# Optimization experiments

Measured on AMD Instinct MI355X. Metric: run time of the kernel, lower is better.

## Reference

```python
import jax, jax.numpy as jnp
import numpy as np

B, T, C = 4, 1024, 768
NH = 12
HD = C // NH  # 64


def setup_inputs() -> dict:
    key = jax.random.key(0)
    k1, k2, k3, k4, k5 = jax.random.split(key, 5)
    s = 0.02
    return {
        "x": jax.random.normal(k1, (B, T, C), dtype=jnp.float32),
        "Wqkv": jax.random.normal(k2, (C, 3 * C), dtype=jnp.float32) * s,
        "bqkv": jax.random.normal(k3, (3 * C,), dtype=jnp.float32) * s,
        "Wproj": jax.random.normal(k4, (C, C), dtype=jnp.float32) * s,
        "bproj": jax.random.normal(k5, (C,), dtype=jnp.float32) * s,
        "start_pos": 0,
    }


def reference(x, Wqkv, bqkv, Wproj, bproj, start_pos):
    # Manual QKV projection (nn.Linear with weight stored as [in, out])
    Bq, Tq, Cq = x.shape
    qkv = x @ Wqkv + bqkv                       # [B, T, 3C]
    q, k, v = jnp.split(qkv, 3, axis=-1)
    q = q.reshape(Bq, Tq, NH, HD)
    k = k.reshape(Bq, Tq, NH, HD)
    v = v.reshape(Bq, Tq, NH, HD)
    # With start_pos=0 the KV-cache write+slice is an identity on k, v.
    att = jnp.einsum("bqhd,bkhd->bhqk", q, k) / jnp.sqrt(jnp.float32(HD))
    causal = jnp.tril(jnp.ones((Tq, Tq), dtype=bool))  # [T, T]
    att = jnp.where(causal[None, None], att, jnp.float32(-jnp.inf))
    att = jax.nn.softmax(att, axis=-1)
    out = jnp.einsum("bhqk,bkhd->bqhd", att, v).reshape(Bq, Tq, Cq)
    return out @ Wproj + bproj
```

## Files before the change

### kernel.cpp

```cpp
#include <hip/hip_runtime.h>


#define BB 4
#define TT 1024
#define CC 768
#define NHH 12
#define HDD 64
#define BHH (BB*NHH)

typedef unsigned short u16;
typedef __attribute__((ext_vector_type(8))) short bf16x8;
typedef __attribute__((ext_vector_type(4))) float f32x4;
typedef __attribute__((ext_vector_type(4))) int i32x4;

__device__ __forceinline__ u16 f2b(float f) {
  unsigned u = __float_as_uint(f);
  u += 0x7fffu + ((u >> 16) & 1u);
  return (u16)(u >> 16);
}
__device__ __forceinline__ unsigned packbf(float lo, float hi) {
  return (__float_as_uint(hi) & 0xffff0000u) | (__float_as_uint(lo) >> 16);
}

__device__ __forceinline__ void gload_lds16(const u16* g, u16* l) {
  __builtin_amdgcn_global_load_lds(
      (const __attribute__((address_space(1))) unsigned int*)g,
      (__attribute__((address_space(3))) unsigned int*)l, 16, 0, 0);
}

__device__ __forceinline__ void tr_body(const float* __restrict__ in, u16* __restrict__ out,
                                        int R, int Cc, int bx, int by, float (*tile)[33]) {
  int c0 = bx * 32, r0 = by * 32;
  int tx = threadIdx.x & 31, ty = threadIdx.x >> 5;
#pragma unroll
  for (int i = 0; i < 32; i += 8)
    tile[ty + i][tx] = in[(r0 + ty + i) * Cc + c0 + tx];
  __syncthreads();
#pragma unroll
  for (int i = 0; i < 32; i += 8)
    out[(c0 + ty + i) * R + r0 + tx] = f2b(tile[tx][ty + i]);
}

__global__ __launch_bounds__(256) void k_prep(const float* __restrict__ x, u16* __restrict__ xb,
                                              const float* __restrict__ Wqkv, u16* __restrict__ Wqkv_t,
                                              const float* __restrict__ Wproj, u16* __restrict__ Wproj_t) {
  __shared__ float tile[32][33];
  int bid = blockIdx.x;
  if (bid < 3072) {
    int i = bid * 256 + threadIdx.x;
    float4 v = ((const float4*)x)[i];
    ushort4 o;
    o.x = f2b(v.x); o.y = f2b(v.y); o.z = f2b(v.z); o.w = f2b(v.w);
    ((ushort4*)xb)[i] = o;
  } else if (bid < 3072 + 1728) {
    int tb = bid - 3072;
    tr_body(Wqkv, Wqkv_t, CC, 3 * CC, tb % 72, tb / 72, tile);
  } else {
    int tb = bid - 4800;
    tr_body(Wproj, Wproj_t, CC, CC, tb % 24, tb / 24, tile);
  }
}

#define GEMM_CORE64(A_, Bt_, m0_, n0_, SMEM)                                      \
  u16* As = (SMEM); u16* Bs = (SMEM) + 8192;                                      \
  int tid = threadIdx.x;                                                          \
  int wave = tid >> 6, lane = tid & 63, quad = lane >> 4, id16 = lane & 15;       \
  int wm = (wave & 1) * 64, wn = (wave >> 1) * 64;                                \
  int srow = tid >> 3;                                                            \
  int schunk = (tid & 7) ^ (srow & 7);                                            \
  const u16* ga = A_ + (m0_ + srow) * CC + schunk * 8;                            \
  const u16* gb = Bt_ + (n0_ + srow) * CC + schunk * 8;                           \
  int xk = id16 & 7;                                                              \
  int off0 = (quad ^ xk) * 8, off1 = ((4 + quad) ^ xk) * 8;                       \
  f32x4 acc[4][4];                                                                \
  _Pragma("unroll") for (int i = 0; i < 4; i++)                                   \
      _Pragma("unroll") for (int j = 0; j < 4; j++) acc[i][j] = (f32x4){0,0,0,0}; \
  for (int k0 = 0; k0 < CC; k0 += 64) {                                           \
    _Pragma("unroll") for (int i = 0; i < 4; i++) {                               \
      gload_lds16(ga + i * 32 * CC + k0, As + i * 2048 + tid * 8);                \
      gload_lds16(gb + i * 32 * CC + k0, Bs + i * 2048 + tid * 8);                \
    }                                                                             \
    __syncthreads();                                                              \
    bf16x8 af[4][2], bfr[4][2];                                                   \
    _Pragma("unroll") for (int i = 0; i < 4; i++) {                               \
      const u16* ar = As + (wm + i * 16 + id16) * 64;                             \
      af[i][0] = *(const bf16x8*)(ar + off0);                                     \
      af[i][1] = *(const bf16x8*)(ar + off1);                                     \
    }                                                                             \
    _Pragma("unroll") for (int j = 0; j < 4; j++) {                               \
      const u16* br = Bs + (wn + j * 16 + id16) * 64;                             \
      bfr[j][0] = *(const bf16x8*)(br + off0);                                    \
      bfr[j][1] = *(const bf16x8*)(br + off1);                                    \
    }                                                                             \
    _Pragma("unroll") for (int i = 0; i < 4; i++)                                 \
        _Pragma("unroll") for (int j = 0; j < 4; j++) {                           \
            acc[i][j] = __builtin_amdgcn_mfma_f32_16x16x32_bf16(af[i][0],         \
                            bfr[j][0], acc[i][j], 0, 0, 0);                       \
            acc[i][j] = __builtin_amdgcn_mfma_f32_16x16x32_bf16(af[i][1],         \
                            bfr[j][1], acc[i][j], 0, 0, 0);                       \
        }                                                                         \
    __syncthreads();                                                              \
  }

__global__ __launch_bounds__(256) void k_qkv(const u16* __restrict__ A, const u16* __restrict__ Bt,
                                             const float* __restrict__ bias,
                                             u16* __restrict__ Qb, u16* __restrict__ Kb,
                                             u16* __restrict__ Vt) {
  __shared__ u16 smem[128 * 136];
  int xcd = blockIdx.x & 7, g = blockIdx.x >> 3;
  int m0 = (xcd + 8 * (g / 18)) * 128, n0 = (g % 18) * 128;
  GEMM_CORE64(A, Bt, m0, n0, smem)
  float bv[4];
#pragma unroll
  for (int j = 0; j < 4; j++) bv[j] = bias[n0 + wn + j * 16 + id16];
  int bi = m0 >> 10, t0 = m0 & 1023;

  if (n0 < 2 * CC) {
    u16* dstb = (n0 < CC) ? Qb : Kb;
    int nrel0 = (n0 < CC) ? n0 : n0 - CC;
#pragma unroll
    for (int i = 0; i < 4; i++)
#pragma unroll
      for (int j = 0; j < 4; j++)
#pragma unroll
        for (int r = 0; r < 4; r++)
          smem[(wm + i * 16 + quad * 4 + r) * 136 + wn + j * 16 + id16] =
              f2b(acc[i][j][r] + bv[j]);
    __syncthreads();
    int m_l = tid >> 1, seg = tid & 1;
    int ng = nrel0 + seg * 64;
    u16* dst = dstb + ((bi * NHH + (ng >> 6)) * TT + t0 + m_l) * HDD;
    const u16* src = smem + m_l * 136 + seg * 64;
#pragma unroll
    for (int w2 = 0; w2 < 8; w2++)
      ((bf16x8*)dst)[w2] = ((const bf16x8*)src)[w2];
  } else {
#pragma unroll
    for (int i = 0; i < 4; i++)
#pragma unroll
      for (int j = 0; j < 4; j++)
#pragma unroll
        for (int r = 0; r < 4; r++)
          smem[(wn + j * 16 + id16) * 136 + wm + i * 16 + quad * 4 + r] =
              f2b(acc[i][j][r] + bv[j]);
    __syncthreads();
    int d2 = tid >> 1, seg = tid & 1;
    int h = (n0 - 2 * CC + d2) >> 6;
    int d = d2 & 63;
    u16* dst = Vt + (((bi * NHH + h) * HDD + d) * TT) + t0 + seg * 64;
    const u16* src = smem + d2 * 136 + seg * 64;
#pragma unroll
    for (int w2 = 0; w2 < 8; w2++)
      ((bf16x8*)dst)[w2] = ((const bf16x8*)src)[w2];
  }
}

__global__ __launch_bounds__(256) void k_proj(const u16* __restrict__ A, const u16* __restrict__ Bt,
                                              const float* __restrict__ bias, float* __restrict__ out) {
  __shared__ u16 smem[16384];
  int xcd = blockIdx.x & 7, g = blockIdx.x >> 3;
  int m0 = (xcd + 8 * (g / 6)) * 128, n0 = (g % 6) * 128;
  GEMM_CORE64(A, Bt, m0, n0, smem)
  float bv[4];
#pragma unroll
  for (int j = 0; j < 4; j++) bv[j] = bias[n0 + wn + j * 16 + id16];
#pragma unroll
  for (int i = 0; i < 4; i++) {
#pragma unroll
    for (int j = 0; j < 4; j++) {
#pragma unroll
      for (int r = 0; r < 4; r++) {
        int m = m0 + wm + i * 16 + quad * 4 + r;
        int n = n0 + wn + j * 16 + id16;
        out[m * CC + n] = acc[i][j][r] + bv[j];
      }
    }
  }
}

__global__ __launch_bounds__(128) void k_attn(const u16* __restrict__ Qb, const u16* __restrict__ Kb,
                                              const u16* __restrict__ Vt, u16* __restrict__ Ob) {
  __shared__ __align__(16) u16 Ks[2][64 * 64];
  __shared__ __align__(16) u16 Vs[2][64 * 64];
  int tid = threadIdx.x;
  int wave = tid >> 6, lane = tid & 63, quad = lane >> 4, id16 = lane & 15;
  int bh = blockIdx.x % BHH, t = 15 - (blockIdx.x / BHH);
  int b = bh / NHH, h = bh % NHH;
  int qw = t * 64 + wave * 32;
  int nch = t + 1;
  const float cexp = 0.125f * 1.44269504088896f;
  bf16x8 bones;
#pragma unroll
  for (int e = 0; e < 8; e++) bones[e] = (short)0x3F80;

  const u16* Kg = Kb + (bh * TT) * HDD;
  const u16* Vg = Vt + (bh * HDD) * TT;
  int srow = tid >> 3;
  int schunk = (tid & 7) ^ (srow & 7);

  int xk = id16 & 7;
  int koff0 = (quad ^ xk) * 8;
  int koff1 = ((quad + 4) ^ xk) * 8;
  int half = (quad & 1) * 4;
  int voff0 = (((quad >> 1)) ^ xk) * 8 + half;
  int voff1 = (((quad >> 1) + 2) ^ xk) * 8 + half;
  int voff2 = (((quad >> 1) + 4) ^ xk) * 8 + half;
  int voff3 = (((quad >> 1) + 6) ^ xk) * 8 + half;

  bf16x8 aq[2][2];
#pragma unroll
  for (int rh = 0; rh < 2; rh++) {
    const u16* Qrow = Qb + (bh * TT + qw + 16 * rh + id16) * HDD;
    aq[rh][0] = *(const bf16x8*)(Qrow + quad * 8);
    aq[rh][1] = *(const bf16x8*)(Qrow + 32 + quad * 8);
  }
  f32x4 o[2][4], ol[2];
#pragma unroll
  for (int rh = 0; rh < 2; rh++) {
    ol[rh] = (f32x4){0,0,0,0};
#pragma unroll
    for (int dt = 0; dt < 4; dt++) o[rh][dt] = (f32x4){0,0,0,0};
  }

#pragma unroll
  for (int i = 0; i < 4; i++) {
    gload_lds16(Kg + (16 * i + srow) * HDD + schunk * 8, Ks[0] + i * 1024 + tid * 8);
    gload_lds16(Vg + (16 * i + srow) * TT + schunk * 8, Vs[0] + i * 1024 + tid * 8);
  }

  for (int c = 0; c < nch; c++) {
    __syncthreads();
    if (c + 1 < nch) {
      int kb = (c + 1) * 64;
      u16* kd = Ks[(c + 1) & 1];
      u16* vd = Vs[(c + 1) & 1];
#pragma unroll
      for (int i = 0; i < 4; i++) {
        gload_lds16(Kg + (kb + 16 * i + srow) * HDD + schunk * 8, kd + i * 1024 + tid * 8);
        gload_lds16(Vg + (16 * i + srow) * TT + kb + schunk * 8, vd + i * 1024 + tid * 8);
      }
    }
    const u16* kbuf = Ks[c & 1];
    const u16* vbuf = Vs[c & 1];
    bool diag = (c == nch - 1);
    int kb = c * 64;

    bf16x8 kf0[4], kf1[4];
#pragma unroll
    for (int kt = 0; kt < 4; kt++) {
      const u16* kr = kbuf + (kt * 16 + id16) * 64;
      kf0[kt] = *(const bf16x8*)(kr + koff0);
      kf1[kt] = *(const bf16x8*)(kr + koff1);
    }
    bf16x8 vf0[4], vf1[4];
#pragma unroll
    for (int dt = 0; dt < 4; dt++) {
      const u16* vr = vbuf + (dt * 16 + id16) * 64;
      uint2 a0 = *(const uint2*)(vr + voff0);
      uint2 a1 = *(const uint2*)(vr + voff1);
      uint2 a2 = *(const uint2*)(vr + voff2);
      uint2 a3 = *(const uint2*)(vr + voff3);
      i32x4 w0, w1;
      w0.x = a0.x; w0.y = a0.y; w0.z = a1.x; w0.w = a1.y;
      w1.x = a2.x; w1.y = a2.y; w1.z = a3.x; w1.w = a3.y;
      vf0[dt] = __builtin_bit_cast(bf16x8, w0);
      vf1[dt] = __builtin_bit_cast(bf16x8, w1);
    }

#pragma unroll
    for (int rh = 0; rh < 2; rh++) {
      f32x4 st[4];
#pragma unroll
      for (int kt = 0; kt < 4; kt++) {
        f32x4 z = {0,0,0,0};
        z = __builtin_amdgcn_mfma_f32_16x16x32_bf16(kf0[kt], aq[rh][0], z, 0, 0, 0);
        st[kt] = __builtin_amdgcn_mfma_f32_16x16x32_bf16(kf1[kt], aq[rh][1], z, 0, 0, 0);
      }
      unsigned pk[4][2];
      if (!diag) {
#pragma unroll
        for (int kt = 0; kt < 4; kt++) {
          pk[kt][0] = packbf(__builtin_amdgcn_exp2f(st[kt][0] * cexp),
                             __builtin_amdgcn_exp2f(st[kt][1] * cexp));
          pk[kt][1] = packbf(__builtin_amdgcn_exp2f(st[kt][2] * cexp),
                             __builtin_amdgcn_exp2f(st[kt][3] * cexp));
        }
      } else {
        int qrow = qw + 16 * rh + id16;
#pragma unroll
        for (int kt = 0; kt < 4; kt++) {
          float pv[4];
#pragma unroll
          for (int r = 0; r < 4; r++) {
            int key = kb + kt * 16 + quad * 4 + r;
            float p = __builtin_amdgcn_exp2f(st[kt][r] * cexp);
            pv[r] = (key <= qrow) ? p : 0.f;
          }
          pk[kt][0] = packbf(pv[0], pv[1]);
          pk[kt][1] = packbf(pv[2], pv[3]);
        }
      }
      i32x4 b0v, b1v;
      b0v.x = (int)pk[0][0]; b0v.y = (int)pk[0][1];
      b0v.z = (int)pk[1][0]; b0v.w = (int)pk[1][1];
      b1v.x = (int)pk[2][0]; b1v.y = (int)pk[2][1];
      b1v.z = (int)pk[3][0]; b1v.w = (int)pk[3][1];
      bf16x8 pf0 = __builtin_bit_cast(bf16x8, b0v);
      bf16x8 pf1 = __builtin_bit_cast(bf16x8, b1v);

#pragma unroll
      for (int dt = 0; dt < 4; dt++) {
        o[rh][dt] = __builtin_amdgcn_mfma_f32_16x16x32_bf16(vf0[dt], pf0, o[rh][dt], 0, 0, 0);
        o[rh][dt] = __builtin_amdgcn_mfma_f32_16x16x32_bf16(vf1[dt], pf1, o[rh][dt], 0, 0, 0);
      }
      ol[rh] = __builtin_amdgcn_mfma_f32_16x16x32_bf16(bones, pf0, ol[rh], 0, 0, 0);
      ol[rh] = __builtin_amdgcn_mfma_f32_16x16x32_bf16(bones, pf1, ol[rh], 0, 0, 0);
    }
  }

#pragma unroll
  for (int rh = 0; rh < 2; rh++) {
    float inv = 1.0f / ol[rh][0];
    int qg = qw + 16 * rh + id16;
    u16* dst = Ob + (b * TT + qg) * CC + h * HDD + quad * 4;
#pragma unroll
    for (int dt = 0; dt < 4; dt++) {
      unsigned lo = ((unsigned)f2b(o[rh][dt][1] * inv) << 16) | f2b(o[rh][dt][0] * inv);
      unsigned hi = ((unsigned)f2b(o[rh][dt][3] * inv) << 16) | f2b(o[rh][dt][2] * inv);
      uint2 pairv; pairv.x = lo; pairv.y = hi;
      *(uint2*)(dst + dt * 16) = pairv;
    }
  }
}

extern "C" void kernel_launch(void* const* d_in, const int* in_sizes, int n_in,
                              void* d_out, int out_size, void* d_ws, size_t ws_size,
                              hipStream_t stream) {
  const float* x     = (const float*)d_in[0];
  const float* Wqkv  = (const float*)d_in[1];
  const float* bqkv  = (const float*)d_in[2];
  const float* Wproj = (const float*)d_in[3];
  const float* bproj = (const float*)d_in[4];
  float* out = (float*)d_out;

  u16* ws = (u16*)d_ws;
  u16* xb      = ws;
  u16* Wqkv_t  = xb + BB * TT * CC;
  u16* Wproj_t = Wqkv_t + 3 * CC * CC;
  u16* Qb      = Wproj_t + CC * CC;
  u16* Kb      = Qb + BHH * TT * HDD;
  u16* Vt      = Kb + BHH * TT * HDD;
  u16* Ob      = Vt + BHH * TT * HDD;

  k_prep<<<3072 + 1728 + 576, 256, 0, stream>>>(x, xb, Wqkv, Wqkv_t, Wproj, Wproj_t);
  k_qkv<<<32 * 18, 256, 0, stream>>>(xb, Wqkv_t, bqkv, Qb, Kb, Vt);
  k_attn<<<16 * BHH, 128, 0, stream>>>(Qb, Kb, Vt, Ob);
  k_proj<<<32 * 6, 256, 0, stream>>>(Ob, Wproj_t, bproj, out);
}
```

Measured before the change: 148.8 us.

## Double-buffer LDS tiles in QKV and projection GEMMs to overlap loads with MFMA

Replaces the single-buffered GEMM main loop with a two-stage ping-pong over two LDS tile pairs. The next K-slice is issued with direct global-to-LDS loads while MFMAs consume the current one, and partial vmcnt waits plus raw s_barrier replace full __syncthreads. This targets the exposed global-load latency per K step. In exchange, LDS per block doubles to 64KB, which may cut the number of resident blocks, and correctness now depends on hand-placed waitcnt counts.

Result: faster. 137.5 us (-7.6%).

```diff
diff --git a/kernel.cpp b/kernel.cpp
--- a/kernel.cpp
+++ b/kernel.cpp
@@ -61,8 +61,36 @@
   }
 }
 
-#define GEMM_CORE64(A_, Bt_, m0_, n0_, SMEM)                                      \
-  u16* As = (SMEM); u16* Bs = (SMEM) + 8192;                                      \
+
+#define STAGE8(k0_, Ad_, Bd_)                                                     \
+  _Pragma("unroll") for (int i_ = 0; i_ < 4; i_++) {                              \
+    gload_lds16(ga + i_ * 32 * CC + (k0_), (Ad_) + i_ * 2048 + tid * 8);          \
+    gload_lds16(gb + i_ * 32 * CC + (k0_), (Bd_) + i_ * 2048 + tid * 8);          \
+  }
+
+#define COMPUTE64(As_, Bs_)                                                       \
+  { bf16x8 af[4][2], bfr[4][2];                                                   \
+    _Pragma("unroll") for (int i = 0; i < 4; i++) {                               \
+      const u16* ar = (As_) + (wm + i * 16 + id16) * 64;                          \
+      af[i][0] = *(const bf16x8*)(ar + off0);                                     \
+      af[i][1] = *(const bf16x8*)(ar + off1);                                     \
+    }                                                                             \
+    _Pragma("unroll") for (int j = 0; j < 4; j++) {                               \
+      const u16* br = (Bs_) + (wn + j * 16 + id16) * 64;                          \
+      bfr[j][0] = *(const bf16x8*)(br + off0);                                    \
+      bfr[j][1] = *(const bf16x8*)(br + off1);                                    \
+    }                                                                             \
+    _Pragma("unroll") for (int i = 0; i < 4; i++)                                 \
+      _Pragma("unroll") for (int j = 0; j < 4; j++) {                             \
+        acc[i][j] = __builtin_amdgcn_mfma_f32_16x16x32_bf16(af[i][0], bfr[j][0],  \
+                                                            acc[i][j], 0, 0, 0);  \
+        acc[i][j] = __builtin_amdgcn_mfma_f32_16x16x32_bf16(af[i][1], bfr[j][1],  \
+                                                            acc[i][j], 0, 0, 0);  \
+      } }
+
+#define GEMM_CORE64_DB(A_, Bt_, m0_, n0_, SMEM)                                   \
+  u16* As0 = (SMEM);          u16* Bs0 = (SMEM) + 8192;                           \
+  u16* As1 = (SMEM) + 16384;  u16* Bs1 = (SMEM) + 24576;                          \
   int tid = threadIdx.x;                                                          \
   int wave = tid >> 6, lane = tid & 63, quad = lane >> 4, id16 = lane & 15;       \
   int wm = (wave & 1) * 64, wn = (wave >> 1) * 64;                                \
@@ -75,41 +103,39 @@
   f32x4 acc[4][4];                                                                \
   _Pragma("unroll") for (int i = 0; i < 4; i++)                                   \
       _Pragma("unroll") for (int j = 0; j < 4; j++) acc[i][j] = (f32x4){0,0,0,0}; \
-  for (int k0 = 0; k0 < CC; k0 += 64) {                                           \
-    _Pragma("unroll") for (int i = 0; i < 4; i++) {                               \
-      gload_lds16(ga + i * 32 * CC + k0, As + i * 2048 + tid * 8);                \
-      gload_lds16(gb + i * 32 * CC + k0, Bs + i * 2048 + tid * 8);                \
+  STAGE8(0, As0, Bs0)                                                             \
+  for (int kk = 0; kk < 6; kk++) {                                                \
+    int kA = kk * 128;                                                            \
+                               \
+    STAGE8(kA + 64, As1, Bs1)                                                     \
+    asm volatile("s_waitcnt vmcnt(8)" ::: "memory");                              \
+    __builtin_amdgcn_s_barrier();                                                 \
+    asm volatile("" ::: "memory");                                                \
+    COMPUTE64(As0, Bs0)                                                           \
+    __builtin_amdgcn_s_barrier();                                                 \
+    asm volatile("" ::: "memory");                                                \
+             \
+    if (kk < 5) {                                                                 \
+      STAGE8(kA + 128, As0, Bs0)                                                  \
+      asm volatile("s_waitcnt vmcnt(8)" ::: "memory");                            \
+    } else {                                                                      \
+      asm volatile("s_waitcnt vmcnt(0)" ::: "memory");                            \
     }                                                                             \
-    __syncthreads();                                                              \
-    bf16x8 af[4][2], bfr[4][2];                                                   \
-    _Pragma("unroll") for (int i = 0; i < 4; i++) {                               \
-      const u16* ar = As + (wm + i * 16 + id16) * 64;                             \
-      af[i][0] = *(const bf16x8*)(ar + off0);                                     \
-      af[i][1] = *(const bf16x8*)(ar + off1);                                     \
-    }                                                                             \
-    _Pragma("unroll") for (int j = 0; j < 4; j++) {                               \
-      const u16* br = Bs + (wn + j * 16 + id16) * 64;                             \
-      bfr[j][0] = *(const bf16x8*)(br + off0);                                    \
-      bfr[j][1] = *(const bf16x8*)(br + off1);                                    \
-    }                                                                             \
-    _Pragma("unroll") for (int i = 0; i < 4; i++)                                 \
-        _Pragma("unroll") for (int j = 0; j < 4; j++) {                           \
-            acc[i][j] = __builtin_amdgcn_mfma_f32_16x16x32_bf16(af[i][0],         \
-                            bfr[j][0], acc[i][j], 0, 0, 0);                       \
-            acc[i][j] = __builtin_amdgcn_mfma_f32_16x16x32_bf16(af[i][1],         \
-                            bfr[j][1], acc[i][j], 0, 0, 0);                       \
-        }                                                                         \
-    __syncthreads();                                                              \
+    __builtin_amdgcn_s_barrier();                                                 \
+    asm volatile("" ::: "memory");                                                \
+    COMPUTE64(As1, Bs1)                                                           \
+    __builtin_amdgcn_s_barrier();                                                 \
+    asm volatile("" ::: "memory");                                                \
   }
 
 __global__ __launch_bounds__(256) void k_qkv(const u16* __restrict__ A, const u16* __restrict__ Bt,
                                              const float* __restrict__ bias,
                                              u16* __restrict__ Qb, u16* __restrict__ Kb,
                                              u16* __restrict__ Vt) {
-  __shared__ u16 smem[128 * 136];
+  __shared__ u16 smem[32768];
   int xcd = blockIdx.x & 7, g = blockIdx.x >> 3;
   int m0 = (xcd + 8 * (g / 18)) * 128, n0 = (g % 18) * 128;
-  GEMM_CORE64(A, Bt, m0, n0, smem)
+  GEMM_CORE64_DB(A, Bt, m0, n0, smem)
   float bv[4];
 #pragma unroll
   for (int j = 0; j < 4; j++) bv[j] = bias[n0 + wn + j * 16 + id16];
@@ -157,10 +183,10 @@
 
 __global__ __launch_bounds__(256) void k_proj(const u16* __restrict__ A, const u16* __restrict__ Bt,
                                               const float* __restrict__ bias, float* __restrict__ out) {
-  __shared__ u16 smem[16384];
+  __shared__ u16 smem[32768];
   int xcd = blockIdx.x & 7, g = blockIdx.x >> 3;
   int m0 = (xcd + 8 * (g / 6)) * 128, n0 = (g % 6) * 128;
-  GEMM_CORE64(A, Bt, m0, n0, smem)
+  GEMM_CORE64_DB(A, Bt, m0, n0, smem)
   float bv[4];
 #pragma unroll
   for (int j = 0; j < 4; j++) bv[j] = bias[n0 + wn + j * 16 + id16];
```
